# Kernel tuning notes

Measured on AMD Instinct MI355X. Metric: run time of the kernel, lower is better.

The kernel has to match this reference:

```python
import jax, jax.numpy as jnp
import numpy as np

ALPHA = 100.0
MARGIN = 5


def _weight_mask(bb, H, W):
    """Analytic per-pixel weight for one sample. bb: (4,2) int, cols = (x, y)."""
    m = MARGIN
    y_min, y_max = bb[:, 1].min(), bb[:, 1].max()
    x_min, x_max = bb[:, 0].min(), bb[:, 0].max()
    ys = jnp.arange(H)[:, None]   # (H,1)
    xs = jnp.arange(W)[None, :]   # (1,W)

    inside = (ys >= y_min) & (ys < y_max) & (xs >= x_min) & (xs < x_max)
    w = jnp.where(inside, ALPHA, 1.0)

    # border region is only weighted when bbox+margin is strictly interior
    cond = (x_min - m > 0) & (x_max + m < W) & (y_min - m > 0) & (y_max + m < H)

    # vertical ramp factor: m inside bbox rows, 1..m on top strip, m..1 on bottom strip, 0 outside
    fy = jnp.where((ys >= y_min) & (ys < y_max), m,
         jnp.where((ys >= y_min - m) & (ys < y_min), ys - (y_min - m) + 1,
         jnp.where((ys >= y_max) & (ys < y_max + m), m - (ys - y_max), 0)))
    fx = jnp.where((xs >= x_min) & (xs < x_max), m,
         jnp.where((xs >= x_min - m) & (xs < x_min), xs - (x_min - m) + 1,
         jnp.where((xs >= x_max) & (xs < x_max + m), m - (xs - x_max), 0)))

    band = (fy > 0) & (fx > 0) & (~inside)
    # linear policy: strips use their own ramp, corners use min of the two ramps
    lin = jnp.minimum(fy, fx).astype(w.dtype) / m * ALPHA
    w = jnp.where(cond & band, lin, w)
    return w  # (H, W)


def setup_inputs() -> dict:
    key = jax.random.key(0)
    k1, k2, k3 = jax.random.split(key, 3)
    B, C, H, W = 32, 3, 512, 512
    x = jax.random.normal(k1, (B, C, H, W), dtype=jnp.float32)
    y = jax.random.normal(k2, (B, C, H, W), dtype=jnp.float32)
    bbox = jax.random.randint(k3, (B, 4, 2), 0, 512, dtype=jnp.int32)
    return {"x": x, "y": y, "bbox": bbox}


def reference(x, y, bbox):
    B, C, H, W = x.shape
    w = jax.vmap(lambda bb: _weight_mask(bb, H, W))(bbox)  # (B,H,W)
    return jnp.mean(jnp.abs(x - y) * w[:, None, :, :])
```

## Files before the change

### kernel.cpp

```cpp
#include <hip/hip_runtime.h>

#define HW_PLANE (512 * 512)
#define TOTAL_PIX (32 * HW_PLANE)
#define TOTAL_QUADS (TOTAL_PIX / 4)
#define N_ELEMS (32 * 3 * HW_PLANE)

__global__ void init_out_kernel(float* out) {
    if (threadIdx.x == 0 && blockIdx.x == 0) out[0] = 0.0f;
}

__global__ __launch_bounds__(256) void mae_bbox_kernel(
    const float* __restrict__ x, const float* __restrict__ y,
    const int* __restrict__ bbox, float* __restrict__ out) {

    const float inv_n = 1.0f / (float)N_ELEMS;
    float acc = 0.0f;

    const int stride = gridDim.x * blockDim.x;
    for (int q = blockIdx.x * blockDim.x + threadIdx.x; q < TOTAL_QUADS; q += stride) {
        const int p   = q << 2;
        const int b   = p >> 18;
        const int rem = p & (HW_PLANE - 1);
        const int h   = rem >> 9;
        const int w0  = rem & 511;

        const int* bb = bbox + (b << 3);
        const int xmin = min(min(bb[0], bb[2]), min(bb[4], bb[6]));
        const int xmax = max(max(bb[0], bb[2]), max(bb[4], bb[6]));
        const int ymin = min(min(bb[1], bb[3]), min(bb[5], bb[7]));
        const int ymax = max(max(bb[1], bb[3]), max(bb[5], bb[7]));

        const bool cond = (xmin > 5) && (xmax < 507) && (ymin > 5) && (ymax < 507);

        const bool inrow = (h >= ymin) && (h < ymax);
        const int fy = inrow ? 5
                     : ((h >= ymin - 5 && h < ymin) ? (h - ymin + 6)
                     : ((h >= ymax && h < ymax + 5) ? (5 - (h - ymax)) : 0));

        float wq[4];
#pragma unroll
        for (int j = 0; j < 4; ++j) {
            const int wx = w0 + j;
            const bool incol = (wx >= xmin) && (wx < xmax);
            const int fx = incol ? 5
                         : ((wx >= xmin - 5 && wx < xmin) ? (wx - xmin + 6)
                         : ((wx >= xmax && wx < xmax + 5) ? (5 - (wx - xmax)) : 0));
            const bool inside = inrow && incol;
            float wv = inside ? 100.0f : 1.0f;
            if (cond && (fy > 0) && (fx > 0) && !inside)
                wv = (float)min(fy, fx) * 20.0f;
            wq[j] = wv;
        }

        const size_t base = (size_t)(b * 3) * HW_PLANE + (size_t)rem;
#pragma unroll
        for (int c = 0; c < 3; ++c) {
            const float4 xv = *reinterpret_cast<const float4*>(x + base + (size_t)c * HW_PLANE);
            const float4 yv = *reinterpret_cast<const float4*>(y + base + (size_t)c * HW_PLANE);
            acc = fmaf(fabsf(xv.x - yv.x), wq[0], acc);
            acc = fmaf(fabsf(xv.y - yv.y), wq[1], acc);
            acc = fmaf(fabsf(xv.z - yv.z), wq[2], acc);
            acc = fmaf(fabsf(xv.w - yv.w), wq[3], acc);
        }
    }

#pragma unroll
    for (int off = 32; off > 0; off >>= 1) acc += __shfl_down(acc, off, 64);

    __shared__ float sred[4];
    const int lane = threadIdx.x & 63;
    const int wid  = threadIdx.x >> 6;
    if (lane == 0) sred[wid] = acc;
    __syncthreads();
    if (threadIdx.x == 0) {
        const float s = sred[0] + sred[1] + sred[2] + sred[3];
        atomicAdd(out, s * inv_n);
    }
}

extern "C" void kernel_launch(void* const* d_in, const int* in_sizes, int n_in,
                              void* d_out, int out_size, void* d_ws, size_t ws_size,
                              hipStream_t stream) {
    const float* x    = (const float*)d_in[0];
    const float* y    = (const float*)d_in[1];
    const int*   bbox = (const int*)d_in[2];
    float* out = (float*)d_out;

    init_out_kernel<<<1, 64, 0, stream>>>(out);

    mae_bbox_kernel<<<2048, 256, 0, stream>>>(x, y, bbox, out);
}
```

Measured before the change: 215.0 us.

## Assign blocks per batch, hoist bbox math, replace atomics with two-pass reduction

Each block now covers a fixed contiguous chunk of one batch image, so the bbox loads and min/max are computed once per block instead of once per quad. The grid-stride loop becomes a fully unrolled four-iteration loop. The global float atomicAdd and the init kernel are replaced by per-block partial sums in workspace plus a single-block finalize kernel, which also gives a deterministic sum order. It still uses two launches and relies on the workspace buffer being large enough.

```diff
diff --git a/kernel.cpp b/kernel.cpp
--- a/kernel.cpp
+++ b/kernel.cpp
@@ -1,36 +1,35 @@
 #include <hip/hip_runtime.h>
 
 #define HW_PLANE (512 * 512)
-#define TOTAL_PIX (32 * HW_PLANE)
-#define TOTAL_QUADS (TOTAL_PIX / 4)
+#define QUADS_PER_BATCH (HW_PLANE / 4)
+#define BLOCKS_PER_BATCH 64
+#define QUADS_PER_BLOCK (QUADS_PER_BATCH / BLOCKS_PER_BATCH)
+#define NBLOCKS (32 * BLOCKS_PER_BATCH)
 #define N_ELEMS (32 * 3 * HW_PLANE)
-
-__global__ void init_out_kernel(float* out) {
-    if (threadIdx.x == 0 && blockIdx.x == 0) out[0] = 0.0f;
-}
 
 __global__ __launch_bounds__(256) void mae_bbox_kernel(
     const float* __restrict__ x, const float* __restrict__ y,
-    const int* __restrict__ bbox, float* __restrict__ out) {
+    const int* __restrict__ bbox, float* __restrict__ ws) {
 
-    const float inv_n = 1.0f / (float)N_ELEMS;
+    const int b     = blockIdx.x >> 6;
+    const int chunk = blockIdx.x & 63;
+
+    const int* bb = bbox + (b << 3);
+    const int xmin = min(min(bb[0], bb[2]), min(bb[4], bb[6]));
+    const int xmax = max(max(bb[0], bb[2]), max(bb[4], bb[6]));
+    const int ymin = min(min(bb[1], bb[3]), min(bb[5], bb[7]));
+    const int ymax = max(max(bb[1], bb[3]), max(bb[5], bb[7]));
+    const bool cond = (xmin > 5) && (xmax < 507) && (ymin > 5) && (ymax < 507);
+
+    const size_t bbase = (size_t)(b * 3) * HW_PLANE;
     float acc = 0.0f;
 
-    const int stride = gridDim.x * blockDim.x;
-    for (int q = blockIdx.x * blockDim.x + threadIdx.x; q < TOTAL_QUADS; q += stride) {
-        const int p   = q << 2;
-        const int b   = p >> 18;
-        const int rem = p & (HW_PLANE - 1);
-        const int h   = rem >> 9;
-        const int w0  = rem & 511;
-
-        const int* bb = bbox + (b << 3);
-        const int xmin = min(min(bb[0], bb[2]), min(bb[4], bb[6]));
-        const int xmax = max(max(bb[0], bb[2]), max(bb[4], bb[6]));
-        const int ymin = min(min(bb[1], bb[3]), min(bb[5], bb[7]));
-        const int ymax = max(max(bb[1], bb[3]), max(bb[5], bb[7]));
-
-        const bool cond = (xmin > 5) && (xmax < 507) && (ymin > 5) && (ymax < 507);
+#pragma unroll
+    for (int it = 0; it < 4; ++it) {
+        const int qb = chunk * QUADS_PER_BLOCK + it * 256 + (int)threadIdx.x;
+        const int p  = qb << 2;
+        const int h  = p >> 9;
+        const int w0 = p & 511;
 
         const bool inrow = (h >= ymin) && (h < ymax);
         const int fy = inrow ? 5
@@ -52,7 +51,7 @@
             wq[j] = wv;
         }
 
-        const size_t base = (size_t)(b * 3) * HW_PLANE + (size_t)rem;
+        const size_t base = bbase + (size_t)p;
 #pragma unroll
         for (int c = 0; c < 3; ++c) {
             const float4 xv = *reinterpret_cast<const float4*>(x + base + (size_t)c * HW_PLANE);
@@ -72,10 +71,27 @@
     const int wid  = threadIdx.x >> 6;
     if (lane == 0) sred[wid] = acc;
     __syncthreads();
-    if (threadIdx.x == 0) {
-        const float s = sred[0] + sred[1] + sred[2] + sred[3];
-        atomicAdd(out, s * inv_n);
-    }
+    if (threadIdx.x == 0)
+        ws[blockIdx.x] = sred[0] + sred[1] + sred[2] + sred[3];
+}
+
+__global__ __launch_bounds__(256) void finalize_kernel(
+    const float* __restrict__ ws, float* __restrict__ out) {
+    float acc = 0.0f;
+#pragma unroll
+    for (int i = 0; i < NBLOCKS / 256; ++i)
+        acc += ws[i * 256 + threadIdx.x];
+
+#pragma unroll
+    for (int off = 32; off > 0; off >>= 1) acc += __shfl_down(acc, off, 64);
+
+    __shared__ float sred[4];
+    const int lane = threadIdx.x & 63;
+    const int wid  = threadIdx.x >> 6;
+    if (lane == 0) sred[wid] = acc;
+    __syncthreads();
+    if (threadIdx.x == 0)
+        out[0] = (sred[0] + sred[1] + sred[2] + sred[3]) * (1.0f / (float)N_ELEMS);
 }
 
 extern "C" void kernel_launch(void* const* d_in, const int* in_sizes, int n_in,
@@ -85,8 +101,8 @@
     const float* y    = (const float*)d_in[1];
     const int*   bbox = (const int*)d_in[2];
     float* out = (float*)d_out;
+    float* ws  = (float*)d_ws;
 
-    init_out_kernel<<<1, 64, 0, stream>>>(out);
-
-    mae_bbox_kernel<<<2048, 256, 0, stream>>>(x, y, bbox, out);
+    mae_bbox_kernel<<<NBLOCKS, 256, 0, stream>>>(x, y, bbox, ws);
+    finalize_kernel<<<1, 256, 0, stream>>>(ws, out);
 }
```

Measured after the change: 213.7 us. No clear change (-0.6%).
